# Kernel tuning notes

Measured on AMD Instinct MI355X. Metric: run time of the kernel, lower is better.

## Reference

```python
import jax, jax.numpy as jnp
import numpy as np


def setup_inputs() -> dict:
    key = jax.random.key(0)
    k1, k2 = jax.random.split(key)
    x = jax.random.normal(k1, (32, 112, 112, 64), dtype=jnp.float32)
    kernels = jax.random.normal(k2, (3, 3, 64, 128), dtype=jnp.float32) * 0.05
    biases = jnp.zeros((128,), dtype=jnp.float32)
    return {"x": x, "kernels": kernels, "biases": biases}


def reference(x, kernels, biases):
    # Stride-1 VALID cross-correlation, NHWC input, HWIO kernel -> NHWC output.
    # Matches the original's per-pixel sum(patch * kernel) over all input channels.
    out = jax.lax.conv_general_dilated(
        x, kernels,
        window_strides=(1, 1),
        padding="VALID",
        dimension_numbers=("NHWC", "HWIO", "NHWC"),
    )
    out = out + biases  # broadcast over (B, H_out, W_out, F)
    return jax.nn.relu(out)  # activation=relu per init_kwargs
```

## Files before the change

kernel.cpp:

```cpp
#include <hip/hip_runtime.h>
#include <hip/hip_bf16.h>

typedef __attribute__((ext_vector_type(4))) float f32x4;
typedef __attribute__((ext_vector_type(8))) short bf16x8;
typedef __attribute__((ext_vector_type(8))) unsigned short u16x8;

#define NB 32
#define HH 112
#define WW 112
#define CIN 64
#define COUT 128
#define HOUT 110
#define WOUT 110
#define NWG 3025

__device__ __forceinline__ unsigned short f2bf(float f) {
  unsigned int x = __float_as_uint(f);
  x += 0x7fffu + ((x >> 16) & 1u);
  return (unsigned short)(x >> 16);
}

__global__ void prepack_b_kernel(const float* __restrict__ kern,
                                 unsigned short* __restrict__ bt) {
  int idx = blockIdx.x * 256 + threadIdx.x;
  if (idx >= 576 * COUT) return;
  int co = idx / 576;
  int k = idx - co * 576;
  bt[idx] = f2bf(kern[k * COUT + co]);
}

template <bool PREPACK>
__global__ __launch_bounds__(512)
void conv_mfma_kernel(const float* __restrict__ x,
                      const void* __restrict__ bsrc,
                      const float* __restrict__ bias,
                      float* __restrict__ out) {
  __shared__ __align__(16) unsigned short As[2][128 * 64];
  __shared__ __align__(16) unsigned short Bs[2][128 * 64];

  const int tid = threadIdx.x;
  const int m0 = blockIdx.x * 128;

  const int sr = tid >> 2;
  const int sc = tid & 3;
  const int m = m0 + sr;
  const int wo = m % WOUT;
  const int t1 = m / WOUT;
  const int ho = t1 % HOUT;
  const int b = t1 / HOUT;
  const float* xrow = x + (((b * HH) + ho) * WW + wo) * CIN + sc * 16;
  const int swzS = (sr & 7) << 4;
  const int awoff0 = sr * 64 + ((((sc * 32) + 0) ^ swzS) >> 1);
  const int awoff1 = sr * 64 + ((((sc * 32) + 16) ^ swzS) >> 1);

  const unsigned short* btrow = nullptr;
  if constexpr (PREPACK) {
    btrow = (const unsigned short*)bsrc + sr * 576 + sc * 16;
  }
  const int bci = tid >> 3;
  const int bco = (tid & 7) * 16;

  const int lane = tid & 63;
  const int wid = tid >> 6;
  const int wm = wid >> 1;
  const int wn = wid & 1;
  const int l16 = lane & 15;
  const int lk = lane >> 4;
  const int swzR = (l16 & 7) << 4;

  const int aroff0 = (wm * 32 + 0 + l16) * 64;
  const int aroff1 = (wm * 32 + 16 + l16) * 64;
  const int broff0 = (wn * 64 + 0 + l16) * 64;
  const int broff1 = (wn * 64 + 16 + l16) * 64;
  const int broff2 = (wn * 64 + 32 + l16) * 64;
  const int broff3 = (wn * 64 + 48 + l16) * 64;

  f32x4 acc[2][4];
#pragma unroll
  for (int i = 0; i < 2; ++i)
#pragma unroll
    for (int j = 0; j < 4; ++j)
      acc[i][j] = (f32x4){0.f, 0.f, 0.f, 0.f};

  {
    f32x4 f0 = *(const f32x4*)(xrow + 0);
    f32x4 f1 = *(const f32x4*)(xrow + 4);
    f32x4 f2 = *(const f32x4*)(xrow + 8);
    f32x4 f3 = *(const f32x4*)(xrow + 12);
    u16x8 v0, v1;
#pragma unroll
    for (int j = 0; j < 4; ++j) {
      v0[j]     = f2bf(f0[j]);
      v0[4 + j] = f2bf(f1[j]);
      v1[j]     = f2bf(f2[j]);
      v1[4 + j] = f2bf(f3[j]);
    }
    *(u16x8*)(As[0] + awoff0) = v0;
    *(u16x8*)(As[0] + awoff1) = v1;
    if constexpr (PREPACK) {
      const u16x8* p = (const u16x8*)btrow;
      *(u16x8*)(Bs[0] + awoff0) = p[0];
      *(u16x8*)(Bs[0] + awoff1) = p[1];
    } else {
      const float* kern = (const float*)bsrc;
      const float* kslab = kern + bci * COUT + bco;
      f32x4 g0 = *(const f32x4*)(kslab + 0);
      f32x4 g1 = *(const f32x4*)(kslab + 4);
      f32x4 g2 = *(const f32x4*)(kslab + 8);
      f32x4 g3 = *(const f32x4*)(kslab + 12);
#pragma unroll
      for (int j = 0; j < 4; ++j) {
        int c0 = bco + j;
        Bs[0][c0 * 64 + (((bci * 2) ^ ((c0 & 7) << 4)) >> 1)] = f2bf(g0[j]);
        int c1 = bco + 4 + j;
        Bs[0][c1 * 64 + (((bci * 2) ^ ((c1 & 7) << 4)) >> 1)] = f2bf(g1[j]);
        int c2 = bco + 8 + j;
        Bs[0][c2 * 64 + (((bci * 2) ^ ((c2 & 7) << 4)) >> 1)] = f2bf(g2[j]);
        int c3 = bco + 12 + j;
        Bs[0][c3 * 64 + (((bci * 2) ^ ((c3 & 7) << 4)) >> 1)] = f2bf(g3[j]);
      }
    }
  }

#pragma unroll
  for (int kk = 0; kk < 9; ++kk) {
    const int cur = kk & 1;
    const int nxt = cur ^ 1;

    f32x4 g0, g1, g2, g3;
    u16x8 bq0, bq1;
    if (kk < 8) {
      const int kn = kk + 1;
      const int kh2 = kn / 3;
      const int kw2 = kn - kh2 * 3;
      const float* src = xrow + (kh2 * WW + kw2) * CIN;
      g0 = *(const f32x4*)(src + 0);
      g1 = *(const f32x4*)(src + 4);
      g2 = *(const f32x4*)(src + 8);
      g3 = *(const f32x4*)(src + 12);
      if constexpr (PREPACK) {
        const u16x8* p = (const u16x8*)(btrow + kn * 64);
        bq0 = p[0];
        bq1 = p[1];
      }
    }

    __syncthreads();

    const unsigned short* Ac = As[cur];
    const unsigned short* Bc = Bs[cur];
#pragma unroll
    for (int ks = 0; ks < 2; ++ks) {
      const int cbs = ((ks * 64 + lk * 16) ^ swzR) >> 1;
      bf16x8 a0 = *(const bf16x8*)(Ac + aroff0 + cbs);
      bf16x8 a1 = *(const bf16x8*)(Ac + aroff1 + cbs);
      bf16x8 b0 = *(const bf16x8*)(Bc + broff0 + cbs);
      bf16x8 b1 = *(const bf16x8*)(Bc + broff1 + cbs);
      bf16x8 b2 = *(const bf16x8*)(Bc + broff2 + cbs);
      bf16x8 b3 = *(const bf16x8*)(Bc + broff3 + cbs);
      acc[0][0] = __builtin_amdgcn_mfma_f32_16x16x32_bf16(a0, b0, acc[0][0], 0, 0, 0);
      acc[0][1] = __builtin_amdgcn_mfma_f32_16x16x32_bf16(a0, b1, acc[0][1], 0, 0, 0);
      acc[0][2] = __builtin_amdgcn_mfma_f32_16x16x32_bf16(a0, b2, acc[0][2], 0, 0, 0);
      acc[0][3] = __builtin_amdgcn_mfma_f32_16x16x32_bf16(a0, b3, acc[0][3], 0, 0, 0);
      acc[1][0] = __builtin_amdgcn_mfma_f32_16x16x32_bf16(a1, b0, acc[1][0], 0, 0, 0);
      acc[1][1] = __builtin_amdgcn_mfma_f32_16x16x32_bf16(a1, b1, acc[1][1], 0, 0, 0);
      acc[1][2] = __builtin_amdgcn_mfma_f32_16x16x32_bf16(a1, b2, acc[1][2], 0, 0, 0);
      acc[1][3] = __builtin_amdgcn_mfma_f32_16x16x32_bf16(a1, b3, acc[1][3], 0, 0, 0);
    }

    if (kk < 8) {
      u16x8 v0, v1;
#pragma unroll
      for (int j = 0; j < 4; ++j) {
        v0[j]     = f2bf(g0[j]);
        v0[4 + j] = f2bf(g1[j]);
        v1[j]     = f2bf(g2[j]);
        v1[4 + j] = f2bf(g3[j]);
      }
      *(u16x8*)(As[nxt] + awoff0) = v0;
      *(u16x8*)(As[nxt] + awoff1) = v1;
      if constexpr (PREPACK) {
        *(u16x8*)(Bs[nxt] + awoff0) = bq0;
        *(u16x8*)(Bs[nxt] + awoff1) = bq1;
      } else {
        const float* kern = (const float*)bsrc;
        const float* kslab = kern + ((kk + 1) * 64 + bci) * COUT + bco;
        f32x4 h0 = *(const f32x4*)(kslab + 0);
        f32x4 h1 = *(const f32x4*)(kslab + 4);
        f32x4 h2 = *(const f32x4*)(kslab + 8);
        f32x4 h3 = *(const f32x4*)(kslab + 12);
#pragma unroll
        for (int j = 0; j < 4; ++j) {
          int c0 = bco + j;
          Bs[nxt][c0 * 64 + (((bci * 2) ^ ((c0 & 7) << 4)) >> 1)] = f2bf(h0[j]);
          int c1 = bco + 4 + j;
          Bs[nxt][c1 * 64 + (((bci * 2) ^ ((c1 & 7) << 4)) >> 1)] = f2bf(h1[j]);
          int c2 = bco + 8 + j;
          Bs[nxt][c2 * 64 + (((bci * 2) ^ ((c2 & 7) << 4)) >> 1)] = f2bf(h2[j]);
          int c3 = bco + 12 + j;
          Bs[nxt][c3 * 64 + (((bci * 2) ^ ((c3 & 7) << 4)) >> 1)] = f2bf(h3[j]);
        }
      }
    }
  }

  const int ncol = wn * 64 + l16;
  const float bv0 = bias[ncol + 0];
  const float bv1 = bias[ncol + 16];
  const float bv2 = bias[ncol + 32];
  const float bv3 = bias[ncol + 48];
  const int mrow0 = m0 + wm * 32 + lk * 4;
#pragma unroll
  for (int mf = 0; mf < 2; ++mf) {
#pragma unroll
    for (int j = 0; j < 4; ++j) {
      const int row = mrow0 + mf * 16 + j;
      float* orow = out + (size_t)row * COUT + ncol;
      orow[0]  = fmaxf(acc[mf][0][j] + bv0, 0.f);
      orow[16] = fmaxf(acc[mf][1][j] + bv1, 0.f);
      orow[32] = fmaxf(acc[mf][2][j] + bv2, 0.f);
      orow[48] = fmaxf(acc[mf][3][j] + bv3, 0.f);
    }
  }
}

extern "C" void kernel_launch(void* const* d_in, const int* in_sizes, int n_in,
                              void* d_out, int out_size, void* d_ws, size_t ws_size,
                              hipStream_t stream) {
  const float* x = (const float*)d_in[0];
  const float* kern = (const float*)d_in[1];
  const float* bias = (const float*)d_in[2];
  float* out = (float*)d_out;

  const size_t bt_bytes = 576 * COUT * sizeof(unsigned short);
  if (d_ws != nullptr && ws_size >= bt_bytes) {
    unsigned short* bt = (unsigned short*)d_ws;
    prepack_b_kernel<<<288, 256, 0, stream>>>(kern, bt);
    conv_mfma_kernel<true><<<NWG, 512, 0, stream>>>(x, (const void*)bt, bias, out);
  } else {
    conv_mfma_kernel<false><<<NWG, 512, 0, stream>>>(x, (const void*)kern, bias, out);
  }
}
```

Measured before the change: 110.4 us.

## Double M tile to 256 rows with XCD-aware block remap and occupancy hint

Raises the output tile from 128x128 to 256x128, so each wave computes a 64x64 sub-tile (16 MFMAs per k-step) and each B tile loaded into LDS is reused across twice as many rows. Workgroup ids are remapped so consecutive tiles land on the same XCD, aiming for better L2 reuse of the overlapping input windows. It adds tail guards for the partial last tile and launch_bounds(512,2) to cap registers. The costs are more LDS (64KB A + 32KB B), a doubled accumulator register footprint and half as many workgroups.

Result: slower. 167.6 us (+51.9%).

```diff
diff --git a/kernel.cpp b/kernel.cpp
--- a/kernel.cpp
+++ b/kernel.cpp
@@ -5,14 +5,16 @@
 typedef __attribute__((ext_vector_type(8))) short bf16x8;
 typedef __attribute__((ext_vector_type(8))) unsigned short u16x8;
 
-#define NB 32
 #define HH 112
 #define WW 112
 #define CIN 64
 #define COUT 128
 #define HOUT 110
 #define WOUT 110
-#define NWG 3025
+#define MTOT 387200
+#define BM 256
+#define NWG 1513
+#define NXCD 8
 
 __device__ __forceinline__ unsigned short f2bf(float f) {
   unsigned int x = __float_as_uint(f);
@@ -30,32 +32,46 @@
 }
 
 template <bool PREPACK>
-__global__ __launch_bounds__(512)
+__global__ __launch_bounds__(512, 2)
 void conv_mfma_kernel(const float* __restrict__ x,
                       const void* __restrict__ bsrc,
                       const float* __restrict__ bias,
                       float* __restrict__ out) {
-  __shared__ __align__(16) unsigned short As[2][128 * 64];
+  __shared__ __align__(16) unsigned short As[2][BM * 64];
   __shared__ __align__(16) unsigned short Bs[2][128 * 64];
 
   const int tid = threadIdx.x;
-  const int m0 = blockIdx.x * 128;
-
-  const int sr = tid >> 2;
-  const int sc = tid & 3;
+
+  const int bid = blockIdx.x;
+  const int q = NWG / NXCD, r = NWG % NXCD;
+  const int xcd = bid % NXCD, i8 = bid / NXCD;
+  const int wg = (xcd < r ? xcd * (q + 1) : r * (q + 1) + (xcd - r) * q) + i8;
+  const int m0 = wg * BM;
+
+  const int sr = tid >> 1;
+  const int sc = tid & 1;
   const int m = m0 + sr;
-  const int wo = m % WOUT;
-  const int t1 = m / WOUT;
+  const int msafe = m < MTOT ? m : (MTOT - 1);
+  const int wo = msafe % WOUT;
+  const int t1 = msafe / WOUT;
   const int ho = t1 % HOUT;
   const int b = t1 / HOUT;
-  const float* xrow = x + (((b * HH) + ho) * WW + wo) * CIN + sc * 16;
+  const float* xrow = x + (((b * HH) + ho) * WW + wo) * CIN + sc * 32;
   const int swzS = (sr & 7) << 4;
-  const int awoff0 = sr * 64 + ((((sc * 32) + 0) ^ swzS) >> 1);
-  const int awoff1 = sr * 64 + ((((sc * 32) + 16) ^ swzS) >> 1);
-
+  const int aw0 = sr * 64 + (((sc * 64) + 0 ^ swzS) >> 1);
+  const int aw1 = sr * 64 + (((sc * 64) + 16 ^ swzS) >> 1);
+  const int aw2 = sr * 64 + (((sc * 64) + 32 ^ swzS) >> 1);
+  const int aw3 = sr * 64 + (((sc * 64) + 48 ^ swzS) >> 1);
+
+  const int sco = tid >> 2;
+  const int cic = (tid & 3) * 16;
   const unsigned short* btrow = nullptr;
+  int bw0 = 0, bw1 = 0;
   if constexpr (PREPACK) {
-    btrow = (const unsigned short*)bsrc + sr * 576 + sc * 16;
+    btrow = (const unsigned short*)bsrc + sco * 576 + cic;
+    const int swzB = (sco & 7) << 4;
+    bw0 = sco * 64 + (((cic * 2) + 0 ^ swzB) >> 1);
+    bw1 = sco * 64 + (((cic * 2) + 16 ^ swzB) >> 1);
   }
   const int bci = tid >> 3;
   const int bco = (tid & 7) * 16;
@@ -68,56 +84,64 @@
   const int lk = lane >> 4;
   const int swzR = (l16 & 7) << 4;
 
-  const int aroff0 = (wm * 32 + 0 + l16) * 64;
-  const int aroff1 = (wm * 32 + 16 + l16) * 64;
-  const int broff0 = (wn * 64 + 0 + l16) * 64;
-  const int broff1 = (wn * 64 + 16 + l16) * 64;
-  const int broff2 = (wn * 64 + 32 + l16) * 64;
-  const int broff3 = (wn * 64 + 48 + l16) * 64;
-
-  f32x4 acc[2][4];
-#pragma unroll
-  for (int i = 0; i < 2; ++i)
+  const int ar0 = (wm * 64 + 0 + l16) * 64;
+  const int ar1 = (wm * 64 + 16 + l16) * 64;
+  const int ar2 = (wm * 64 + 32 + l16) * 64;
+  const int ar3 = (wm * 64 + 48 + l16) * 64;
+  const int br0 = (wn * 64 + 0 + l16) * 64;
+  const int br1 = (wn * 64 + 16 + l16) * 64;
+  const int br2 = (wn * 64 + 32 + l16) * 64;
+  const int br3 = (wn * 64 + 48 + l16) * 64;
+
+  f32x4 acc[4][4];
+#pragma unroll
+  for (int i = 0; i < 4; ++i)
 #pragma unroll
     for (int j = 0; j < 4; ++j)
       acc[i][j] = (f32x4){0.f, 0.f, 0.f, 0.f};
 
   {
-    f32x4 f0 = *(const f32x4*)(xrow + 0);
-    f32x4 f1 = *(const f32x4*)(xrow + 4);
-    f32x4 f2 = *(const f32x4*)(xrow + 8);
-    f32x4 f3 = *(const f32x4*)(xrow + 12);
-    u16x8 v0, v1;
+    f32x4 g0 = *(const f32x4*)(xrow + 0);
+    f32x4 g1 = *(const f32x4*)(xrow + 4);
+    f32x4 g2 = *(const f32x4*)(xrow + 8);
+    f32x4 g3 = *(const f32x4*)(xrow + 12);
+    f32x4 g4 = *(const f32x4*)(xrow + 16);
+    f32x4 g5 = *(const f32x4*)(xrow + 20);
+    f32x4 g6 = *(const f32x4*)(xrow + 24);
+    f32x4 g7 = *(const f32x4*)(xrow + 28);
+    u16x8 v0, v1, v2, v3;
 #pragma unroll
     for (int j = 0; j < 4; ++j) {
-      v0[j]     = f2bf(f0[j]);
-      v0[4 + j] = f2bf(f1[j]);
-      v1[j]     = f2bf(f2[j]);
-      v1[4 + j] = f2bf(f3[j]);
-    }
-    *(u16x8*)(As[0] + awoff0) = v0;
-    *(u16x8*)(As[0] + awoff1) = v1;
+      v0[j] = f2bf(g0[j]); v0[4 + j] = f2bf(g1[j]);
+      v1[j] = f2bf(g2[j]); v1[4 + j] = f2bf(g3[j]);
+      v2[j] = f2bf(g4[j]); v2[4 + j] = f2bf(g5[j]);
+      v3[j] = f2bf(g6[j]); v3[4 + j] = f2bf(g7[j]);
+    }
+    *(u16x8*)(As[0] + aw0) = v0;
+    *(u16x8*)(As[0] + aw1) = v1;
+    *(u16x8*)(As[0] + aw2) = v2;
+    *(u16x8*)(As[0] + aw3) = v3;
     if constexpr (PREPACK) {
       const u16x8* p = (const u16x8*)btrow;
-      *(u16x8*)(Bs[0] + awoff0) = p[0];
-      *(u16x8*)(Bs[0] + awoff1) = p[1];
+      *(u16x8*)(Bs[0] + bw0) = p[0];
+      *(u16x8*)(Bs[0] + bw1) = p[1];
     } else {
       const float* kern = (const float*)bsrc;
       const float* kslab = kern + bci * COUT + bco;
-      f32x4 g0 = *(const f32x4*)(kslab + 0);
-      f32x4 g1 = *(const f32x4*)(kslab + 4);
-      f32x4 g2 = *(const f32x4*)(kslab + 8);
-      f32x4 g3 = *(const f32x4*)(kslab + 12);
+      f32x4 h0 = *(const f32x4*)(kslab + 0);
+      f32x4 h1 = *(const f32x4*)(kslab + 4);
+      f32x4 h2 = *(const f32x4*)(kslab + 8);
+      f32x4 h3 = *(const f32x4*)(kslab + 12);
 #pragma unroll
       for (int j = 0; j < 4; ++j) {
         int c0 = bco + j;
-        Bs[0][c0 * 64 + (((bci * 2) ^ ((c0 & 7) << 4)) >> 1)] = f2bf(g0[j]);
+        Bs[0][c0 * 64 + (((bci * 2) ^ ((c0 & 7) << 4)) >> 1)] = f2bf(h0[j]);
         int c1 = bco + 4 + j;
-        Bs[0][c1 * 64 + (((bci * 2) ^ ((c1 & 7) << 4)) >> 1)] = f2bf(g1[j]);
+        Bs[0][c1 * 64 + (((bci * 2) ^ ((c1 & 7) << 4)) >> 1)] = f2bf(h1[j]);
         int c2 = bco + 8 + j;
-        Bs[0][c2 * 64 + (((bci * 2) ^ ((c2 & 7) << 4)) >> 1)] = f2bf(g2[j]);
+        Bs[0][c2 * 64 + (((bci * 2) ^ ((c2 & 7) << 4)) >> 1)] = f2bf(h2[j]);
         int c3 = bco + 12 + j;
-        Bs[0][c3 * 64 + (((bci * 2) ^ ((c3 & 7) << 4)) >> 1)] = f2bf(g3[j]);
+        Bs[0][c3 * 64 + (((bci * 2) ^ ((c3 & 7) << 4)) >> 1)] = f2bf(h3[j]);
       }
     }
   }
@@ -127,7 +151,7 @@
     const int cur = kk & 1;
     const int nxt = cur ^ 1;
 
-    f32x4 g0, g1, g2, g3;
+    f32x4 g0, g1, g2, g3, g4, g5, g6, g7;
     u16x8 bq0, bq1;
     if (kk < 8) {
       const int kn = kk + 1;
@@ -138,6 +162,10 @@
       g1 = *(const f32x4*)(src + 4);
       g2 = *(const f32x4*)(src + 8);
       g3 = *(const f32x4*)(src + 12);
+      g4 = *(const f32x4*)(src + 16);
+      g5 = *(const f32x4*)(src + 20);
+      g6 = *(const f32x4*)(src + 24);
+      g7 = *(const f32x4*)(src + 28);
       if constexpr (PREPACK) {
         const u16x8* p = (const u16x8*)(btrow + kn * 64);
         bq0 = p[0];
@@ -152,12 +180,14 @@
 #pragma unroll
     for (int ks = 0; ks < 2; ++ks) {
       const int cbs = ((ks * 64 + lk * 16) ^ swzR) >> 1;
-      bf16x8 a0 = *(const bf16x8*)(Ac + aroff0 + cbs);
-      bf16x8 a1 = *(const bf16x8*)(Ac + aroff1 + cbs);
-      bf16x8 b0 = *(const bf16x8*)(Bc + broff0 + cbs);
-      bf16x8 b1 = *(const bf16x8*)(Bc + broff1 + cbs);
-      bf16x8 b2 = *(const bf16x8*)(Bc + broff2 + cbs);
-      bf16x8 b3 = *(const bf16x8*)(Bc + broff3 + cbs);
+      bf16x8 a0 = *(const bf16x8*)(Ac + ar0 + cbs);
+      bf16x8 a1 = *(const bf16x8*)(Ac + ar1 + cbs);
+      bf16x8 a2 = *(const bf16x8*)(Ac + ar2 + cbs);
+      bf16x8 a3 = *(const bf16x8*)(Ac + ar3 + cbs);
+      bf16x8 b0 = *(const bf16x8*)(Bc + br0 + cbs);
+      bf16x8 b1 = *(const bf16x8*)(Bc + br1 + cbs);
+      bf16x8 b2 = *(const bf16x8*)(Bc + br2 + cbs);
+      bf16x8 b3 = *(const bf16x8*)(Bc + br3 + cbs);
       acc[0][0] = __builtin_amdgcn_mfma_f32_16x16x32_bf16(a0, b0, acc[0][0], 0, 0, 0);
       acc[0][1] = __builtin_amdgcn_mfma_f32_16x16x32_bf16(a0, b1, acc[0][1], 0, 0, 0);
       acc[0][2] = __builtin_amdgcn_mfma_f32_16x16x32_bf16(a0, b2, acc[0][2], 0, 0, 0);
@@ -166,22 +196,32 @@
       acc[1][1] = __builtin_amdgcn_mfma_f32_16x16x32_bf16(a1, b1, acc[1][1], 0, 0, 0);
       acc[1][2] = __builtin_amdgcn_mfma_f32_16x16x32_bf16(a1, b2, acc[1][2], 0, 0, 0);
       acc[1][3] = __builtin_amdgcn_mfma_f32_16x16x32_bf16(a1, b3, acc[1][3], 0, 0, 0);
+      acc[2][0] = __builtin_amdgcn_mfma_f32_16x16x32_bf16(a2, b0, acc[2][0], 0, 0, 0);
+      acc[2][1] = __builtin_amdgcn_mfma_f32_16x16x32_bf16(a2, b1, acc[2][1], 0, 0, 0);
+      acc[2][2] = __builtin_amdgcn_mfma_f32_16x16x32_bf16(a2, b2, acc[2][2], 0, 0, 0);
+      acc[2][3] = __builtin_amdgcn_mfma_f32_16x16x32_bf16(a2, b3, acc[2][3], 0, 0, 0);
+      acc[3][0] = __builtin_amdgcn_mfma_f32_16x16x32_bf16(a3, b0, acc[3][0], 0, 0, 0);
+      acc[3][1] = __builtin_amdgcn_mfma_f32_16x16x32_bf16(a3, b1, acc[3][1], 0, 0, 0);
+      acc[3][2] = __builtin_amdgcn_mfma_f32_16x16x32_bf16(a3, b2, acc[3][2], 0, 0, 0);
+      acc[3][3] = __builtin_amdgcn_mfma_f32_16x16x32_bf16(a3, b3, acc[3][3], 0, 0, 0);
     }
 
     if (kk < 8) {
-      u16x8 v0, v1;
+      u16x8 v0, v1, v2, v3;
 #pragma unroll
       for (int j = 0; j < 4; ++j) {
-        v0[j]     = f2bf(g0[j]);
-        v0[4 + j] = f2bf(g1[j]);
-        v1[j]     = f2bf(g2[j]);
-        v1[4 + j] = f2bf(g3[j]);
-      }
-      *(u16x8*)(As[nxt] + awoff0) = v0;
-      *(u16x8*)(As[nxt] + awoff1) = v1;
+        v0[j] = f2bf(g0[j]); v0[4 + j] = f2bf(g1[j]);
+        v1[j] = f2bf(g2[j]); v1[4 + j] = f2bf(g3[j]);
+        v2[j] = f2bf(g4[j]); v2[4 + j] = f2bf(g5[j]);
+        v3[j] = f2bf(g6[j]); v3[4 + j] = f2bf(g7[j]);
+      }
+      *(u16x8*)(As[nxt] + aw0) = v0;
+      *(u16x8*)(As[nxt] + aw1) = v1;
+      *(u16x8*)(As[nxt] + aw2) = v2;
+      *(u16x8*)(As[nxt] + aw3) = v3;
       if constexpr (PREPACK) {
-        *(u16x8*)(Bs[nxt] + awoff0) = bq0;
-        *(u16x8*)(Bs[nxt] + awoff1) = bq1;
+        *(u16x8*)(Bs[nxt] + bw0) = bq0;
+        *(u16x8*)(Bs[nxt] + bw1) = bq1;
       } else {
         const float* kern = (const float*)bsrc;
         const float* kslab = kern + ((kk + 1) * 64 + bci) * COUT + bco;
@@ -209,17 +249,19 @@
   const float bv1 = bias[ncol + 16];
   const float bv2 = bias[ncol + 32];
   const float bv3 = bias[ncol + 48];
-  const int mrow0 = m0 + wm * 32 + lk * 4;
-#pragma unroll
-  for (int mf = 0; mf < 2; ++mf) {
+#pragma unroll
+  for (int i = 0; i < 4; ++i) {
+    const int rbase = m0 + wm * 64 + i * 16 + lk * 4;
 #pragma unroll
     for (int j = 0; j < 4; ++j) {
-      const int row = mrow0 + mf * 16 + j;
-      float* orow = out + (size_t)row * COUT + ncol;
-      orow[0]  = fmaxf(acc[mf][0][j] + bv0, 0.f);
-      orow[16] = fmaxf(acc[mf][1][j] + bv1, 0.f);
-      orow[32] = fmaxf(acc[mf][2][j] + bv2, 0.f);
-      orow[48] = fmaxf(acc[mf][3][j] + bv3, 0.f);
+      const int row = rbase + j;
+      if (row < MTOT) {
+        float* orow = out + (size_t)row * COUT + ncol;
+        orow[0]  = fmaxf(acc[i][0][j] + bv0, 0.f);
+        orow[16] = fmaxf(acc[i][1][j] + bv1, 0.f);
+        orow[32] = fmaxf(acc[i][2][j] + bv2, 0.f);
+        orow[48] = fmaxf(acc[i][3][j] + bv3, 0.f);
+      }
     }
   }
 }
```
